# Performance work log

Hardware: AMD Instinct MI355X
Metric: run time of the kernel (lower is better)

## Reference

```python
import jax, jax.numpy as jnp
import numpy as np

D_MODEL = 256
D_INNER = 512      # expand(2) * d_model
D_STATE = 16
DT_RANK = 16       # ceil(256/16)
D_CONV = 4
DEPTH = 2


def _silu(x):
    return x * jax.nn.sigmoid(x)


def _selective_scan(u, dt, A, B, C, D):
    # u,dt: [b,l,d]; A: [d,n]; B,C: [b,l,n]; D: [d]
    dA = jnp.einsum('bld,dn->bldn', dt, A)
    dBu = jnp.einsum('bld,bld,bln->bldn', dt, u, B)
    # torch: F.pad(dA[:,1:], last-l-dim one zero).flip(1).cumsum(1).exp().flip(1)
    dA_shift = jnp.concatenate([dA[:, 1:], jnp.zeros_like(dA[:, :1])], axis=1)
    dAc = jnp.exp(jnp.cumsum(dA_shift[:, ::-1], axis=1)[:, ::-1])
    x = jnp.cumsum(dBu * dAc, axis=1) / (dAc + 1e-12)
    y = jnp.einsum('bldn,bln->bld', x, C)
    return y + u * D


def _block(x, p):
    # x: [b,l,d_model]
    in_w, conv_w, conv_b, xproj_w, dt_w, dt_b, A_log, Dp, out_w = p
    xr = jnp.einsum('bld,ed->ble', x, in_w)           # [b,l,2*d_inner]
    xx, res = jnp.split(xr, 2, axis=-1)
    # causal depthwise conv1d (padding d_conv-1 then truncate == left-pad)
    xc = jax.lax.conv_general_dilated(
        xx.transpose(0, 2, 1), conv_w, window_strides=(1,),
        padding=[(D_CONV - 1, 0)], feature_group_count=D_INNER,
        dimension_numbers=('NCH', 'OIH', 'NCH')) + conv_b[None, :, None]
    xx = _silu(xc.transpose(0, 2, 1))                 # [b,l,d_inner]
    x_dbl = jnp.einsum('bld,ed->ble', xx, xproj_w)
    delta = x_dbl[..., :DT_RANK]
    B = x_dbl[..., DT_RANK:DT_RANK + D_STATE]
    C = x_dbl[..., DT_RANK + D_STATE:]
    delta = jax.nn.softplus(jnp.einsum('blr,dr->bld', delta, dt_w) + dt_b)
    A = -jnp.exp(A_log)
    y = _selective_scan(xx, delta, A, B, C, Dp)
    y = y * _silu(res)
    return jnp.einsum('bld,od->blo', y, out_w)


def _model1(x, params):
    for i in range(DEPTH):
        x = _block(x, tuple(q[i] for q in params))
    return x


def setup_inputs() -> dict:
    key = jax.random.key(0)
    ks = jax.random.split(key, 8)

    def nrm(k, shape, scale):
        return (jax.random.normal(k, shape) * scale).astype(jnp.float32)

    x0 = jax.random.normal(ks[0], (4, D_MODEL, 256, 256), jnp.float32)
    in_w = nrm(ks[1], (DEPTH, 2 * D_INNER, D_MODEL), 0.02)
    conv_w = nrm(ks[2], (DEPTH, D_INNER, 1, D_CONV), 0.1)
    conv_b = jnp.zeros((DEPTH, D_INNER), jnp.float32)
    xproj_w = nrm(ks[3], (DEPTH, DT_RANK + 2 * D_STATE, D_INNER), 0.02)
    dt_w = nrm(ks[4], (DEPTH, D_INNER, DT_RANK), 0.05)
    dt_b = jnp.full((DEPTH, D_INNER), -4.0, jnp.float32)  # small deltas for stability
    A_log = jnp.tile(jnp.log(jnp.arange(1, D_STATE + 1, dtype=jnp.float32))[None, None, :],
                     (DEPTH, D_INNER, 1))
    Dp = jnp.ones((DEPTH, D_INNER), jnp.float32)
    out_w = nrm(ks[5], (DEPTH, D_MODEL, D_INNER), 0.02)
    return dict(x0=x0, in_w=in_w, conv_w=conv_w, conv_b=conv_b, xproj_w=xproj_w,
                dt_w=dt_w, dt_b=dt_b, A_log=A_log, Dp=Dp, out_w=out_w)


def reference(x0, in_w, conv_w, conv_b, xproj_w, dt_w, dt_b, A_log, Dp, out_w):
    params = (in_w, conv_w, conv_b, xproj_w, dt_w, dt_b, A_log, Dp, out_w)
    # h-axis: pool over w, mamba over length h (weights shared with w pass)
    x_h = x0.mean(axis=3)                                        # [b,c,h]
    xm_h = _model1(x_h.transpose(0, 2, 1), params)               # [b,h,c]
    xm_h = xm_h.transpose(0, 2, 1)[..., None] * x0               # [b,c,h,w]
    # w-axis: pool over h of gated map, mamba over length w
    x_w = xm_h.mean(axis=2)                                      # [b,c,w]
    xm_w = _model1(x_w.transpose(0, 2, 1), params)               # [b,w,c]
    return xm_w.transpose(0, 2, 1)[:, :, None, :] * x0           # [b,c,h,w]
```

## Files before the change

kernel.cpp:

```cpp
#include <hip/hip_runtime.h>
#include <math.h>

#define BSZ 4
#define DM 256
#define HH 256
#define WW 256
#define LL 256
#define DI 512
#define NBL (BSZ * LL)

__global__ __launch_bounds__(256) void k_mean_w(const float* __restrict__ x0,
                                                float* __restrict__ xseq) {
    int wave = (blockIdx.x * blockDim.x + threadIdx.x) >> 6;
    int lane = threadIdx.x & 63;
    int b = wave >> 16;
    int d = (wave >> 8) & 255;
    int h = wave & 255;
    const float4* row = (const float4*)(x0 + (size_t)wave * WW);
    float4 v = row[lane];
    float s = v.x + v.y + v.z + v.w;
#pragma unroll
    for (int m = 32; m >= 1; m >>= 1) s += __shfl_xor(s, m);
    if (lane == 0) xseq[((size_t)(b * LL) + h) * DM + d] = s * (1.0f / WW);
}

__global__ __launch_bounds__(256) void k_gemm_nt32(const float* __restrict__ A,
                                                   const float* __restrict__ Bw,
                                                   float* __restrict__ C,
                                                   int M, int N, int K) {
    __shared__ float As[16][32];
    __shared__ float Bs[16][64];
    int tid = threadIdx.x;
    int tx = tid & 15, ty = tid >> 4;
    int n0 = blockIdx.x * 64;
    int m0 = blockIdx.y * 32;
    int lr = tid >> 2;
    int lk = (tid & 3) * 4;

    float acc[2][4];
#pragma unroll
    for (int i = 0; i < 2; ++i)
#pragma unroll
        for (int j = 0; j < 4; ++j) acc[i][j] = 0.0f;

    for (int k0 = 0; k0 < K; k0 += 16) {
        float4 bv = *(const float4*)(Bw + (size_t)(n0 + lr) * K + k0 + lk);
        float4 av;
        if (tid < 128) av = *(const float4*)(A + (size_t)(m0 + lr) * K + k0 + lk);
        __syncthreads();
        Bs[lk + 0][lr] = bv.x; Bs[lk + 1][lr] = bv.y; Bs[lk + 2][lr] = bv.z; Bs[lk + 3][lr] = bv.w;
        if (tid < 128) {
            As[lk + 0][lr] = av.x; As[lk + 1][lr] = av.y; As[lk + 2][lr] = av.z; As[lk + 3][lr] = av.w;
        }
        __syncthreads();
#pragma unroll
        for (int kk = 0; kk < 16; ++kk) {
            float a0 = As[kk][ty * 2 + 0];
            float a1 = As[kk][ty * 2 + 1];
            float4 bf = *(const float4*)(&Bs[kk][tx << 2]);
            float bb[4] = {bf.x, bf.y, bf.z, bf.w};
#pragma unroll
            for (int j = 0; j < 4; ++j) {
                acc[0][j] = fmaf(a0, bb[j], acc[0][j]);
                acc[1][j] = fmaf(a1, bb[j], acc[1][j]);
            }
        }
    }
#pragma unroll
    for (int i = 0; i < 2; ++i)
#pragma unroll
        for (int j = 0; j < 4; ++j)
            C[(size_t)(m0 + ty * 2 + i) * N + n0 + (tx << 2) + j] = acc[i][j];
}

__global__ __launch_bounds__(256) void k_mid(const float* __restrict__ xz,
                                             const float* __restrict__ cw,
                                             const float* __restrict__ cb,
                                             const float* __restrict__ xpw,
                                             float* __restrict__ xx,
                                             float* __restrict__ xdbl) {
    __shared__ float xs[DI];
    __shared__ float pr[256];
    int bl = blockIdx.x;
    int b = bl >> 8, l = bl & 255;
    int tid = threadIdx.x;

#pragma unroll
    for (int c = 0; c < 2; ++c) {
        int d = tid + 256 * c;
        float4 w4 = *(const float4*)(cw + d * 4);
        float wk[4] = {w4.x, w4.y, w4.z, w4.w};
        float acc = cb[d];
#pragma unroll
        for (int k = 0; k < 4; ++k) {
            int ls = l + k - 3;
            float v = (ls >= 0) ? xz[((size_t)(b * LL + ls)) * (2 * DI) + d] : 0.0f;
            acc = fmaf(wk[k], v, acc);
        }
        float v = acc / (1.0f + expf(-acc));
        xs[d] = v;
        xx[(size_t)bl * DI + d] = v;
    }
    __syncthreads();

    int e = tid >> 2, c = tid & 3;
    float a = 0.0f;
    if (e < 48) {
        const float4* xv = (const float4*)(xs + c * 128);
        const float4* wv = (const float4*)(xpw + (size_t)e * DI + c * 128);
#pragma unroll 8
        for (int q = 0; q < 32; ++q) {
            float4 x4 = xv[q], p4 = wv[q];
            a = fmaf(x4.x, p4.x, a);
            a = fmaf(x4.y, p4.y, a);
            a = fmaf(x4.z, p4.z, a);
            a = fmaf(x4.w, p4.w, a);
        }
    }
    pr[tid] = a;
    __syncthreads();
    if (tid < 48)
        xdbl[(size_t)bl * 48 + tid] = pr[4 * tid] + pr[4 * tid + 1] + pr[4 * tid + 2] + pr[4 * tid + 3];
}

__global__ __launch_bounds__(256) void k_scan(const float* __restrict__ xx,
                                              const float* __restrict__ xdbl,
                                              const float* __restrict__ xz,
                                              const float* __restrict__ Alog,
                                              const float* __restrict__ Dp,
                                              const float* __restrict__ dtw,
                                              const float* __restrict__ dtb,
                                              float* __restrict__ yg) {
    __shared__ float yred[4][LL];
    __shared__ float us[LL];
    int tid = threadIdx.x;
    int lane = tid & 63, w = tid >> 6;
    int seq = blockIdx.x;
    int d = seq & (DI - 1), b = seq >> 9;
    int l0 = lane * 4;

    const float* xd0 = xdbl + ((size_t)(b * LL) + l0) * 48;

    const float* wr = dtw + d * 16;
    float4 w0 = *(const float4*)(wr + 0);
    float4 w1 = *(const float4*)(wr + 4);
    float4 w2 = *(const float4*)(wr + 8);
    float4 w3 = *(const float4*)(wr + 12);
    float bias = dtb[d];

    float dt[4], u[4], dtu[4], P[4];
#pragma unroll
    for (int i = 0; i < 4; ++i) {
        const float* xr = xd0 + i * 48;
        float4 a0 = *(const float4*)(xr + 0);
        float4 a1 = *(const float4*)(xr + 4);
        float4 a2 = *(const float4*)(xr + 8);
        float4 a3 = *(const float4*)(xr + 12);
        float acc = bias;
        acc = fmaf(a0.x, w0.x, acc); acc = fmaf(a0.y, w0.y, acc);
        acc = fmaf(a0.z, w0.z, acc); acc = fmaf(a0.w, w0.w, acc);
        acc = fmaf(a1.x, w1.x, acc); acc = fmaf(a1.y, w1.y, acc);
        acc = fmaf(a1.z, w1.z, acc); acc = fmaf(a1.w, w1.w, acc);
        acc = fmaf(a2.x, w2.x, acc); acc = fmaf(a2.y, w2.y, acc);
        acc = fmaf(a2.z, w2.z, acc); acc = fmaf(a2.w, w2.w, acc);
        acc = fmaf(a3.x, w3.x, acc); acc = fmaf(a3.y, w3.y, acc);
        acc = fmaf(a3.z, w3.z, acc); acc = fmaf(a3.w, w3.w, acc);
        dt[i] = (acc > 20.0f) ? acc : log1pf(expf(acc));
        u[i] = xx[((size_t)(b * LL) + l0 + i) * DI + d];
        dtu[i] = dt[i] * u[i];
    }

    P[0] = dt[0]; P[1] = P[0] + dt[1]; P[2] = P[1] + dt[2]; P[3] = P[2] + dt[3];
    float s = P[3];
#pragma unroll
    for (int off = 1; off < 64; off <<= 1) {
        float t = __shfl_up(s, off);
        if (lane >= off) s += t;
    }
    float base = s - P[3];
    float dt_end = __shfl(s, 63);
    float Dtc[4];
#pragma unroll
    for (int i = 0; i < 4; ++i) Dtc[i] = P[i] + base;

    if (w == 0) {
#pragma unroll
        for (int i = 0; i < 4; ++i) us[l0 + i] = u[i];
    }

    float4 Al = *(const float4*)(Alog + d * 16 + 4 * w);
    float A[4] = {-expf(Al.x), -expf(Al.y), -expf(Al.z), -expf(Al.w)};
    float Bv[4][4], Cv[4][4];
#pragma unroll
    for (int i = 0; i < 4; ++i) {
        float4 bq = *(const float4*)(xd0 + i * 48 + 16 + 4 * w);
        float4 cq = *(const float4*)(xd0 + i * 48 + 32 + 4 * w);
        Bv[i][0] = bq.x; Bv[i][1] = bq.y; Bv[i][2] = bq.z; Bv[i][3] = bq.w;
        Cv[i][0] = cq.x; Cv[i][1] = cq.y; Cv[i][2] = cq.z; Cv[i][3] = cq.w;
    }

    float y[4] = {0.0f, 0.0f, 0.0f, 0.0f};
#pragma unroll
    for (int c = 0; c < 4; ++c) {
        float Ac = A[c];
        float dAc[4], t[4];
#pragma unroll
        for (int i = 0; i < 4; ++i) {
            dAc[i] = expf(Ac * (dt_end - Dtc[i]));
            t[i] = dtu[i] * Bv[i][c] * dAc[i];
        }
        float p0 = t[0], p1 = p0 + t[1], p2 = p1 + t[2], p3 = p2 + t[3];
        float ss = p3;
#pragma unroll
        for (int off = 1; off < 64; off <<= 1) {
            float tt = __shfl_up(ss, off);
            if (lane >= off) ss += tt;
        }
        float baseT = ss - p3;
        y[0] += (p0 + baseT) / (dAc[0] + 1e-12f) * Cv[0][c];
        y[1] += (p1 + baseT) / (dAc[1] + 1e-12f) * Cv[1][c];
        y[2] += (p2 + baseT) / (dAc[2] + 1e-12f) * Cv[2][c];
        y[3] += (p3 + baseT) / (dAc[3] + 1e-12f) * Cv[3][c];
    }
#pragma unroll
    for (int i = 0; i < 4; ++i) yred[w][l0 + i] = y[i];
    __syncthreads();

    int l = tid;
    float ysum = yred[0][l] + yred[1][l] + yred[2][l] + yred[3][l];
    float yv = fmaf(us[l], Dp[d], ysum);
    float res = xz[((size_t)(b * LL) + l) * (2 * DI) + DI + d];
    yg[((size_t)(b * LL) + l) * DI + d] = yv * (res / (1.0f + expf(-res)));
}

__global__ __launch_bounds__(256) void k_fuse_mean_h(const float* __restrict__ m,
                                                     const float* __restrict__ x0,
                                                     float* __restrict__ xw) {
    int bd = blockIdx.x;
    int b = bd >> 8, d = bd & 255;
    int w = threadIdx.x;
    __shared__ float ms[HH];
    ms[w] = m[((size_t)(b * LL) + w) * DM + d];
    __syncthreads();
    const float* xrow = x0 + (size_t)bd * HH * WW;
    float a0 = 0.0f, a1 = 0.0f, a2 = 0.0f, a3 = 0.0f;
    for (int h = 0; h < HH; h += 8) {
        float xv[8];
#pragma unroll
        for (int j = 0; j < 8; ++j) xv[j] = xrow[(size_t)(h + j) * WW + w];
        a0 = fmaf(ms[h + 0], xv[0], a0);
        a1 = fmaf(ms[h + 1], xv[1], a1);
        a2 = fmaf(ms[h + 2], xv[2], a2);
        a3 = fmaf(ms[h + 3], xv[3], a3);
        a0 = fmaf(ms[h + 4], xv[4], a0);
        a1 = fmaf(ms[h + 5], xv[5], a1);
        a2 = fmaf(ms[h + 6], xv[6], a2);
        a3 = fmaf(ms[h + 7], xv[7], a3);
    }
    float acc = (a0 + a1) + (a2 + a3);
    xw[((size_t)(b * LL) + w) * DM + d] = acc * (1.0f / HH);
}

__global__ __launch_bounds__(256) void k_final(const float* __restrict__ mw,
                                               const float* __restrict__ x0,
                                               float* __restrict__ out) {
    __shared__ float ms[WW];
    int bd = blockIdx.x;
    int b = bd >> 8, d = bd & 255;
    int tid = threadIdx.x;
    ms[tid] = mw[((size_t)(b * LL) + tid) * DM + d];
    __syncthreads();

    int w4 = tid & 63;
    int hq = tid >> 6;
    float4 mv = *(const float4*)(ms + (w4 << 2));
    const float4* xin = (const float4*)(x0 + (size_t)bd * HH * WW);
    float4* oout = (float4*)(out + (size_t)bd * HH * WW);
#pragma unroll 4
    for (int hi = 0; hi < 64; ++hi) {
        int h = hi * 4 + hq;
        size_t idx = (size_t)h * 64 + w4;
        float4 xv = xin[idx];
        float4 o;
        o.x = mv.x * xv.x;
        o.y = mv.y * xv.y;
        o.z = mv.z * xv.z;
        o.w = mv.w * xv.w;
        oout[idx] = o;
    }
}

extern "C" void kernel_launch(void* const* d_in, const int* in_sizes, int n_in,
                              void* d_out, int out_size, void* d_ws, size_t ws_size,
                              hipStream_t stream) {
    const float* x0     = (const float*)d_in[0];
    const float* in_w   = (const float*)d_in[1];
    const float* conv_w = (const float*)d_in[2];
    const float* conv_b = (const float*)d_in[3];
    const float* xproj_w= (const float*)d_in[4];
    const float* dt_w   = (const float*)d_in[5];
    const float* dt_b   = (const float*)d_in[6];
    const float* A_log  = (const float*)d_in[7];
    const float* Dp     = (const float*)d_in[8];
    const float* out_w  = (const float*)d_in[9];
    float* out = (float*)d_out;

    float* S0   = (float*)d_ws;
    float* S1   = S0 + 262144;
    float* S2   = S1 + 262144;
    float* xz   = S2 + 262144;
    float* xx   = xz + 1048576;
    float* xdbl = xx + 524288;
    float* yg   = xdbl + 49152;

    auto run_block = [&](const float* in, float* outb, int layer) {
        k_gemm_nt32<<<dim3((2 * DI) / 64, NBL / 32), 256, 0, stream>>>(
            in, in_w + (size_t)layer * 2 * DI * DM, xz, NBL, 2 * DI, DM);
        k_mid<<<NBL, 256, 0, stream>>>(
            xz, conv_w + (size_t)layer * DI * 4, conv_b + (size_t)layer * DI,
            xproj_w + (size_t)layer * 48 * DI, xx, xdbl);
        k_scan<<<BSZ * DI, 256, 0, stream>>>(
            xx, xdbl, xz, A_log + (size_t)layer * DI * 16, Dp + (size_t)layer * DI,
            dt_w + (size_t)layer * DI * 16, dt_b + (size_t)layer * DI, yg);
        k_gemm_nt32<<<dim3(DM / 64, NBL / 32), 256, 0, stream>>>(
            yg, out_w + (size_t)layer * DM * DI, outb, NBL, DM, DI);
    };

    k_mean_w<<<65536, 256, 0, stream>>>(x0, S0);
    run_block(S0, S1, 0);
    run_block(S1, S2, 1);
    k_fuse_mean_h<<<BSZ * DM, 256, 0, stream>>>(S2, x0, S0);
    run_block(S0, S1, 0);
    run_block(S1, S2, 1);
    k_final<<<BSZ * DM, 256, 0, stream>>>(S2, x0, out);
}
```

Measured before the change: 571.1 us.

## Fold out_proj of layer 0 into in_proj of layer 1 and transpose scan output

Precomputes the product of layer-1 in_proj and layer-0 out_proj weights inside the mean-pooling kernel, removing one GEMM per model pass and the intermediate activation round-trip. The scan writes its gated output transposed so a new TN GEMM can read it contiguously. GEMM shared-memory tiles are padded and stores vectorized, and the mean kernel processes multiple rows per wave. The weight fold changes floating-point summation order slightly and adds a small weight GEMM per call.

```diff
diff --git a/kernel.cpp b/kernel.cpp
--- a/kernel.cpp
+++ b/kernel.cpp
@@ -3,33 +3,93 @@
 
 #define BSZ 4
 #define DM 256
-#define HH 256
-#define WW 256
 #define LL 256
 #define DI 512
 #define NBL (BSZ * LL)
 
-__global__ __launch_bounds__(256) void k_mean_w(const float* __restrict__ x0,
-                                                float* __restrict__ xseq) {
-    int wave = (blockIdx.x * blockDim.x + threadIdx.x) >> 6;
-    int lane = threadIdx.x & 63;
-    int b = wave >> 16;
-    int d = (wave >> 8) & 255;
-    int h = wave & 255;
-    const float4* row = (const float4*)(x0 + (size_t)wave * WW);
-    float4 v = row[lane];
-    float s = v.x + v.y + v.z + v.w;
-#pragma unroll
-    for (int m = 32; m >= 1; m >>= 1) s += __shfl_xor(s, m);
-    if (lane == 0) xseq[((size_t)(b * LL) + h) * DM + d] = s * (1.0f / WW);
+__global__ __launch_bounds__(256) void k_meanw_prep(const float* __restrict__ x0,
+                                                    const float* __restrict__ in_w1,
+                                                    const float* __restrict__ out_w0,
+                                                    float* __restrict__ S0,
+                                                    float* __restrict__ Wf) {
+    __shared__ float smem[1664];
+    int bl = blockIdx.x;
+    int tid = threadIdx.x;
+    if (bl < 1024) {
+        int wv = tid >> 6, lane = tid & 63;
+        const float4* x4 = (const float4*)x0;
+        int rbase = bl * 256 + wv * 64;
+        for (int i0 = 0; i0 < 64; i0 += 4) {
+            float s[4];
+#pragma unroll
+            for (int j = 0; j < 4; ++j) {
+                float4 v = x4[(size_t)(rbase + i0 + j) * 64 + lane];
+                s[j] = (v.x + v.y) + (v.z + v.w);
+            }
+#pragma unroll
+            for (int j = 0; j < 4; ++j) {
+#pragma unroll
+                for (int m = 32; m >= 1; m >>= 1) s[j] += __shfl_xor(s[j], m);
+            }
+            if (lane == 0) {
+#pragma unroll
+                for (int j = 0; j < 4; ++j) {
+                    int rr = rbase + i0 + j;
+                    int b = rr >> 16, d = (rr >> 8) & 255, h = rr & 255;
+                    S0[((size_t)(b * LL) + h) * DM + d] = s[j] * (1.0f / 256.0f);
+                }
+            }
+        }
+    } else {
+        float* As = smem;
+        float* Bs = smem + 576;
+        int t = bl - 1024;
+        int e0 = (t >> 4) * 32, k0c = (t & 15) * 32;
+        int tx = tid & 15, ty = tid >> 4;
+        float acc00 = 0.f, acc01 = 0.f, acc10 = 0.f, acc11 = 0.f;
+        for (int dm0 = 0; dm0 < 256; dm0 += 16) {
+            float4 v;
+            if (tid < 128) {
+                int r = tid >> 2, q = tid & 3;
+                v = *(const float4*)(in_w1 + (size_t)(e0 + r) * 256 + dm0 + 4 * q);
+                __syncthreads();
+                As[(4 * q + 0) * 36 + r] = v.x;
+                As[(4 * q + 1) * 36 + r] = v.y;
+                As[(4 * q + 2) * 36 + r] = v.z;
+                As[(4 * q + 3) * 36 + r] = v.w;
+            } else {
+                int idx = tid - 128;
+                int r = idx >> 3, q = idx & 7;
+                v = *(const float4*)(out_w0 + (size_t)(dm0 + r) * 512 + k0c + 4 * q);
+                __syncthreads();
+                Bs[r * 36 + 4 * q + 0] = v.x;
+                Bs[r * 36 + 4 * q + 1] = v.y;
+                Bs[r * 36 + 4 * q + 2] = v.z;
+                Bs[r * 36 + 4 * q + 3] = v.w;
+            }
+            __syncthreads();
+#pragma unroll
+            for (int kk = 0; kk < 16; ++kk) {
+                float2 a = *(const float2*)(As + kk * 36 + 2 * ty);
+                float2 b = *(const float2*)(Bs + kk * 36 + 2 * tx);
+                acc00 = fmaf(a.x, b.x, acc00);
+                acc01 = fmaf(a.x, b.y, acc01);
+                acc10 = fmaf(a.y, b.x, acc10);
+                acc11 = fmaf(a.y, b.y, acc11);
+            }
+        }
+        float* c0 = Wf + (size_t)(e0 + 2 * ty) * 512 + k0c + 2 * tx;
+        c0[0] = acc00; c0[1] = acc01;
+        c0[512] = acc10; c0[513] = acc11;
+    }
 }
 
 __global__ __launch_bounds__(256) void k_gemm_nt32(const float* __restrict__ A,
                                                    const float* __restrict__ Bw,
                                                    float* __restrict__ C,
                                                    int M, int N, int K) {
-    __shared__ float As[16][32];
-    __shared__ float Bs[16][64];
+    __shared__ float As[16][36];
+    __shared__ float Bs[16][68];
     int tid = threadIdx.x;
     int tx = tid & 15, ty = tid >> 4;
     int n0 = blockIdx.x * 64;
@@ -55,22 +115,92 @@
         __syncthreads();
 #pragma unroll
         for (int kk = 0; kk < 16; ++kk) {
-            float a0 = As[kk][ty * 2 + 0];
-            float a1 = As[kk][ty * 2 + 1];
-            float4 bf = *(const float4*)(&Bs[kk][tx << 2]);
-            float bb[4] = {bf.x, bf.y, bf.z, bf.w};
-#pragma unroll
-            for (int j = 0; j < 4; ++j) {
-                acc[0][j] = fmaf(a0, bb[j], acc[0][j]);
-                acc[1][j] = fmaf(a1, bb[j], acc[1][j]);
-            }
-        }
-    }
+            float2 a = *(const float2*)(&As[kk][2 * ty]);
+            float4 bf = *(const float4*)(&Bs[kk][4 * tx]);
+            acc[0][0] = fmaf(a.x, bf.x, acc[0][0]);
+            acc[0][1] = fmaf(a.x, bf.y, acc[0][1]);
+            acc[0][2] = fmaf(a.x, bf.z, acc[0][2]);
+            acc[0][3] = fmaf(a.x, bf.w, acc[0][3]);
+            acc[1][0] = fmaf(a.y, bf.x, acc[1][0]);
+            acc[1][1] = fmaf(a.y, bf.y, acc[1][1]);
+            acc[1][2] = fmaf(a.y, bf.z, acc[1][2]);
+            acc[1][3] = fmaf(a.y, bf.w, acc[1][3]);
+        }
+    }
+#pragma unroll
+    for (int i = 0; i < 2; ++i) {
+        float4 o;
+        o.x = acc[i][0]; o.y = acc[i][1]; o.z = acc[i][2]; o.w = acc[i][3];
+        *(float4*)(C + (size_t)(m0 + 2 * ty + i) * N + n0 + 4 * tx) = o;
+    }
+}
+
+__global__ __launch_bounds__(256) void k_gemm_tn(const float* __restrict__ At,
+                                                 const float* __restrict__ B,
+                                                 float* __restrict__ C,
+                                                 int ldc) {
+    __shared__ float As[16 * 36];
+    __shared__ float Bs[16 * 68];
+    int tid = threadIdx.x;
+    int tx = tid & 15, ty = tid >> 4;
+    int n0 = blockIdx.x * 64;
+    int m0 = blockIdx.y * 32;
+    int b = m0 >> 8, l0 = m0 & 255;
+
+    float acc[2][4];
 #pragma unroll
     for (int i = 0; i < 2; ++i)
 #pragma unroll
-        for (int j = 0; j < 4; ++j)
-            C[(size_t)(m0 + ty * 2 + i) * N + n0 + (tx << 2) + j] = acc[i][j];
+        for (int j = 0; j < 4; ++j) acc[i][j] = 0.0f;
+
+    for (int d0 = 0; d0 < 512; d0 += 16) {
+        float4 va, vb1, vb2;
+        if (tid < 128) {
+            int r = tid >> 3, q = tid & 7;
+            va = *(const float4*)(At + ((size_t)(b * 512 + d0 + r)) * 256 + l0 + 4 * q);
+        } else {
+            int idx = tid - 128;
+            int nr = idx >> 1, q = idx & 1;
+            const float* bp = B + (size_t)(n0 + nr) * 512 + d0 + 8 * q;
+            vb1 = *(const float4*)(bp);
+            vb2 = *(const float4*)(bp + 4);
+        }
+        __syncthreads();
+        if (tid < 128) {
+            int r = tid >> 3, q = tid & 7;
+            *(float4*)(As + r * 36 + 4 * q) = va;
+        } else {
+            int idx = tid - 128, nr = idx >> 1, q = idx & 1;
+            Bs[(8 * q + 0) * 68 + nr] = vb1.x;
+            Bs[(8 * q + 1) * 68 + nr] = vb1.y;
+            Bs[(8 * q + 2) * 68 + nr] = vb1.z;
+            Bs[(8 * q + 3) * 68 + nr] = vb1.w;
+            Bs[(8 * q + 4) * 68 + nr] = vb2.x;
+            Bs[(8 * q + 5) * 68 + nr] = vb2.y;
+            Bs[(8 * q + 6) * 68 + nr] = vb2.z;
+            Bs[(8 * q + 7) * 68 + nr] = vb2.w;
+        }
+        __syncthreads();
+#pragma unroll
+        for (int kk = 0; kk < 16; ++kk) {
+            float2 a = *(const float2*)(As + kk * 36 + 2 * ty);
+            float4 bf = *(const float4*)(Bs + kk * 68 + 4 * tx);
+            acc[0][0] = fmaf(a.x, bf.x, acc[0][0]);
+            acc[0][1] = fmaf(a.x, bf.y, acc[0][1]);
+            acc[0][2] = fmaf(a.x, bf.z, acc[0][2]);
+            acc[0][3] = fmaf(a.x, bf.w, acc[0][3]);
+            acc[1][0] = fmaf(a.y, bf.x, acc[1][0]);
+            acc[1][1] = fmaf(a.y, bf.y, acc[1][1]);
+            acc[1][2] = fmaf(a.y, bf.z, acc[1][2]);
+            acc[1][3] = fmaf(a.y, bf.w, acc[1][3]);
+        }
+    }
+#pragma unroll
+    for (int i = 0; i < 2; ++i) {
+        float4 o;
+        o.x = acc[i][0]; o.y = acc[i][1]; o.z = acc[i][2]; o.w = acc[i][3];
+        *(float4*)(C + (size_t)(m0 + 2 * ty + i) * ldc + n0 + 4 * tx) = o;
+    }
 }
 
 __global__ __launch_bounds__(256) void k_mid(const float* __restrict__ xz,
@@ -89,13 +219,12 @@
     for (int c = 0; c < 2; ++c) {
         int d = tid + 256 * c;
         float4 w4 = *(const float4*)(cw + d * 4);
-        float wk[4] = {w4.x, w4.y, w4.z, w4.w};
         float acc = cb[d];
 #pragma unroll
         for (int k = 0; k < 4; ++k) {
             int ls = l + k - 3;
-            float v = (ls >= 0) ? xz[((size_t)(b * LL + ls)) * (2 * DI) + d] : 0.0f;
-            acc = fmaf(wk[k], v, acc);
+            float v = (ls >= 0) ? xz[((size_t)(b * LL + ls)) * 1024 + d] : 0.0f;
+            acc = fmaf(((const float*)&w4)[k], v, acc);
         }
         float v = acc / (1.0f + expf(-acc));
         xs[d] = v;
@@ -103,14 +232,14 @@
     }
     __syncthreads();
 
-    int e = tid >> 2, c = tid & 3;
+    int e = tid >> 2, c2 = tid & 3;
     float a = 0.0f;
     if (e < 48) {
-        const float4* xv = (const float4*)(xs + c * 128);
-        const float4* wv = (const float4*)(xpw + (size_t)e * DI + c * 128);
+        const float4* xv4 = (const float4*)(xs + c2 * 128);
+        const float4* wv4 = (const float4*)(xpw + (size_t)e * DI + c2 * 128);
 #pragma unroll 8
         for (int q = 0; q < 32; ++q) {
-            float4 x4 = xv[q], p4 = wv[q];
+            float4 x4 = xv4[q], p4 = wv4[q];
             a = fmaf(x4.x, p4.x, a);
             a = fmaf(x4.y, p4.y, a);
             a = fmaf(x4.z, p4.z, a);
@@ -130,7 +259,7 @@
                                               const float* __restrict__ Dp,
                                               const float* __restrict__ dtw,
                                               const float* __restrict__ dtb,
-                                              float* __restrict__ yg) {
+                                              float* __restrict__ ygT) {
     __shared__ float yred[4][LL];
     __shared__ float us[LL];
     int tid = threadIdx.x;
@@ -140,7 +269,6 @@
     int l0 = lane * 4;
 
     const float* xd0 = xdbl + ((size_t)(b * LL) + l0) * 48;
-
     const float* wr = dtw + d * 16;
     float4 w0 = *(const float4*)(wr + 0);
     float4 w1 = *(const float4*)(wr + 4);
@@ -199,7 +327,7 @@
         Cv[i][0] = cq.x; Cv[i][1] = cq.y; Cv[i][2] = cq.z; Cv[i][3] = cq.w;
     }
 
-    float y[4] = {0.0f, 0.0f, 0.0f, 0.0f};
+    float y[4] = {0.f, 0.f, 0.f, 0.f};
 #pragma unroll
     for (int c = 0; c < 4; ++c) {
         float Ac = A[c];
@@ -229,8 +357,8 @@
     int l = tid;
     float ysum = yred[0][l] + yred[1][l] + yred[2][l] + yred[3][l];
     float yv = fmaf(us[l], Dp[d], ysum);
-    float res = xz[((size_t)(b * LL) + l) * (2 * DI) + DI + d];
-    yg[((size_t)(b * LL) + l) * DI + d] = yv * (res / (1.0f + expf(-res)));
+    float res = xz[((size_t)(b * LL) + l) * 1024 + DI + d];
+    ygT[(size_t)seq * LL + l] = yv * (res / (1.0f + expf(-res)));
 }
 
 __global__ __launch_bounds__(256) void k_fuse_mean_h(const float* __restrict__ m,
@@ -239,15 +367,15 @@
     int bd = blockIdx.x;
     int b = bd >> 8, d = bd & 255;
     int w = threadIdx.x;
-    __shared__ float ms[HH];
+    __shared__ float ms[LL];
     ms[w] = m[((size_t)(b * LL) + w) * DM + d];
     __syncthreads();
-    const float* xrow = x0 + (size_t)bd * HH * WW;
+    const float* xrow = x0 + (size_t)bd * 65536;
     float a0 = 0.0f, a1 = 0.0f, a2 = 0.0f, a3 = 0.0f;
-    for (int h = 0; h < HH; h += 8) {
+    for (int h = 0; h < 256; h += 8) {
         float xv[8];
 #pragma unroll
-        for (int j = 0; j < 8; ++j) xv[j] = xrow[(size_t)(h + j) * WW + w];
+        for (int j = 0; j < 8; ++j) xv[j] = xrow[(size_t)(h + j) * 256 + w];
         a0 = fmaf(ms[h + 0], xv[0], a0);
         a1 = fmaf(ms[h + 1], xv[1], a1);
         a2 = fmaf(ms[h + 2], xv[2], a2);
@@ -258,13 +386,13 @@
         a3 = fmaf(ms[h + 7], xv[7], a3);
     }
     float acc = (a0 + a1) + (a2 + a3);
-    xw[((size_t)(b * LL) + w) * DM + d] = acc * (1.0f / HH);
+    xw[((size_t)(b * LL) + w) * DM + d] = acc * (1.0f / 256.0f);
 }
 
 __global__ __launch_bounds__(256) void k_final(const float* __restrict__ mw,
                                                const float* __restrict__ x0,
                                                float* __restrict__ out) {
-    __shared__ float ms[WW];
+    __shared__ float ms[LL];
     int bd = blockIdx.x;
     int b = bd >> 8, d = bd & 255;
     int tid = threadIdx.x;
@@ -274,8 +402,8 @@
     int w4 = tid & 63;
     int hq = tid >> 6;
     float4 mv = *(const float4*)(ms + (w4 << 2));
-    const float4* xin = (const float4*)(x0 + (size_t)bd * HH * WW);
-    float4* oout = (float4*)(out + (size_t)bd * HH * WW);
+    const float4* xin = (const float4*)(x0 + (size_t)bd * 65536);
+    float4* oout = (float4*)(out + (size_t)bd * 65536);
 #pragma unroll 4
     for (int hi = 0; hi < 64; ++hi) {
         int h = hi * 4 + hq;
@@ -293,44 +421,43 @@
 extern "C" void kernel_launch(void* const* d_in, const int* in_sizes, int n_in,
                               void* d_out, int out_size, void* d_ws, size_t ws_size,
                               hipStream_t stream) {
-    const float* x0     = (const float*)d_in[0];
-    const float* in_w   = (const float*)d_in[1];
-    const float* conv_w = (const float*)d_in[2];
-    const float* conv_b = (const float*)d_in[3];
-    const float* xproj_w= (const float*)d_in[4];
-    const float* dt_w   = (const float*)d_in[5];
-    const float* dt_b   = (const float*)d_in[6];
-    const float* A_log  = (const float*)d_in[7];
-    const float* Dp     = (const float*)d_in[8];
-    const float* out_w  = (const float*)d_in[9];
+    const float* x0      = (const float*)d_in[0];
+    const float* in_w    = (const float*)d_in[1];
+    const float* conv_w  = (const float*)d_in[2];
+    const float* conv_b  = (const float*)d_in[3];
+    const float* xproj_w = (const float*)d_in[4];
+    const float* dt_w    = (const float*)d_in[5];
+    const float* dt_b    = (const float*)d_in[6];
+    const float* A_log   = (const float*)d_in[7];
+    const float* Dp      = (const float*)d_in[8];
+    const float* out_w   = (const float*)d_in[9];
     float* out = (float*)d_out;
 
     float* S0   = (float*)d_ws;
-    float* S1   = S0 + 262144;
-    float* S2   = S1 + 262144;
-    float* xz   = S2 + 262144;
+    float* Sout = S0 + 262144;
+    float* Wf   = Sout + 262144;
+    float* xz   = Wf + 524288;
     float* xx   = xz + 1048576;
     float* xdbl = xx + 524288;
-    float* yg   = xdbl + 49152;
-
-    auto run_block = [&](const float* in, float* outb, int layer) {
-        k_gemm_nt32<<<dim3((2 * DI) / 64, NBL / 32), 256, 0, stream>>>(
-            in, in_w + (size_t)layer * 2 * DI * DM, xz, NBL, 2 * DI, DM);
-        k_mid<<<NBL, 256, 0, stream>>>(
-            xz, conv_w + (size_t)layer * DI * 4, conv_b + (size_t)layer * DI,
-            xproj_w + (size_t)layer * 48 * DI, xx, xdbl);
-        k_scan<<<BSZ * DI, 256, 0, stream>>>(
-            xx, xdbl, xz, A_log + (size_t)layer * DI * 16, Dp + (size_t)layer * DI,
-            dt_w + (size_t)layer * DI * 16, dt_b + (size_t)layer * DI, yg);
-        k_gemm_nt32<<<dim3(DM / 64, NBL / 32), 256, 0, stream>>>(
-            yg, out_w + (size_t)layer * DM * DI, outb, NBL, DM, DI);
+    float* ygT  = xdbl + 49152;
+
+    const float* out_w1 = out_w + 131072;
+
+    auto run_model = [&](const float* inb, float* outb) {
+        k_gemm_nt32<<<dim3(16, 32), 256, 0, stream>>>(inb, in_w, xz, NBL, 1024, 256);
+        k_mid<<<NBL, 256, 0, stream>>>(xz, conv_w, conv_b, xproj_w, xx, xdbl);
+        k_scan<<<BSZ * DI, 256, 0, stream>>>(xx, xdbl, xz, A_log, Dp, dt_w, dt_b, ygT);
+        k_gemm_tn<<<dim3(16, 32), 256, 0, stream>>>(ygT, Wf, xz, 1024);
+        k_mid<<<NBL, 256, 0, stream>>>(xz, conv_w + 2048, conv_b + 512,
+                                       xproj_w + 24576, xx, xdbl);
+        k_scan<<<BSZ * DI, 256, 0, stream>>>(xx, xdbl, xz, A_log + 8192, Dp + 512,
+                                             dt_w + 8192, dt_b + 512, ygT);
+        k_gemm_tn<<<dim3(4, 32), 256, 0, stream>>>(ygT, out_w1, outb, 256);
     };
 
-    k_mean_w<<<65536, 256, 0, stream>>>(x0, S0);
-    run_block(S0, S1, 0);
-    run_block(S1, S2, 1);
-    k_fuse_mean_h<<<BSZ * DM, 256, 0, stream>>>(S2, x0, S0);
-    run_block(S0, S1, 0);
-    run_block(S1, S2, 1);
-    k_final<<<BSZ * DM, 256, 0, stream>>>(S2, x0, out);
-}
+    k_meanw_prep<<<1536, 256, 0, stream>>>(x0, in_w + 262144, out_w, S0, Wf);
+    run_model(S0, Sout);
+    k_fuse_mean_h<<<NBL, 256, 0, stream>>>(Sout, x0, S0);
+    run_model(S0, Sout);
+    k_final<<<NBL, 256, 0, stream>>>(Sout, x0, out);
+}
```

Result: faster. 554.1 us (-3.0%).
